# Kernel tuning notes

Measured on AMD Instinct MI355X. Metric: run time of the kernel, lower is better.

## Reference

```python
import jax, jax.numpy as jnp
import numpy as np

BETA = 0.25


def setup_inputs() -> dict:
    key = jax.random.key(0)
    k1, k2 = jax.random.split(key)
    z = jax.random.normal(k1, (16, 2048, 256), dtype=jnp.float32)
    # n_q=4 codebooks, each [n_e=2048, e_dim=256]; xavier-ish scale
    W = jax.random.normal(k2, (4, 2048, 256), dtype=jnp.float32) * 0.05
    return {"z": z, "W": W}


def reference(z, W):
    """Residual VQ forward (p=1.0, eval-mode math). Returns (z_q, loss, indices)."""
    n_q, n_e, e_dim = W.shape
    lead = z.shape[:-1]
    flat_shape = (-1, e_dim)

    residual = z
    cumulative_q = jnp.zeros_like(z)
    losses = []
    idx_list = []
    for k in range(n_q):
        Wk = W[k]  # [n_e, e_dim]
        flat = residual.reshape(flat_shape)  # [N, e_dim]
        dist = (
            jnp.sum(flat * flat, axis=1, keepdims=True)
            - 2.0 * (flat @ Wk.T)
            + jnp.sum(Wk * Wk, axis=1)[None, :]
        )
        idx = jnp.argmin(dist, axis=1)  # [N]
        # one_hot @ Wk is mathematically a gather of codebook rows
        q = Wk[idx].reshape(residual.shape)
        # commit + beta*codebook; both are (residual.detach() - q)^2.mean(-1)
        diff = jax.lax.stop_gradient(residual) - q
        losses.append((1.0 + BETA) * jnp.mean(diff * diff, axis=-1))
        cumulative_q = cumulative_q + q
        residual = residual - q
        idx_list.append(idx.reshape(*lead, 1))

    # straight-through: gradient of z_q flows only to z
    z_q = z + jax.lax.stop_gradient(cumulative_q - z)
    total_loss = jnp.mean(jnp.stack(losses, axis=0).mean(axis=0))
    indices = jnp.concatenate(idx_list, axis=-1)  # [..., n_q]
    return z_q, total_loss, indices
```

## Files before the change

kernel.cpp:

```cpp
#include <hip/hip_runtime.h>
#include <cstdint>
#include <math.h>
#include <float.h>

#define N_Q   4
#define NROWS 32768
#define EDIM  256
#define NE    2048
#define NCT   64
#define TM    64
#define NTHREADS 256

#define ZQ_SIZE  (NROWS * EDIM)
#define LOSS_OFF ZQ_SIZE
#define IDX_OFF  (ZQ_SIZE + 1)

#define TAU 0.012f

typedef __attribute__((ext_vector_type(8))) _Float16 f16x8;
typedef __attribute__((ext_vector_type(4))) float    f32x4;

union F8 { _Float16 h[8]; f16x8 v; };

__device__ __forceinline__ float np_block128_sq(const float* __restrict__ p) {
    #pragma clang fp contract(off)
    float r[8];
    #pragma unroll
    for (int j = 0; j < 8; ++j) { float v = p[j]; r[j] = v * v; }
    for (int i = 8; i < 128; i += 8) {
        #pragma unroll
        for (int j = 0; j < 8; ++j) { float v = p[i + j]; float sq = v * v; r[j] = r[j] + sq; }
    }
    return ((r[0] + r[1]) + (r[2] + r[3])) + ((r[4] + r[5]) + (r[6] + r[7]));
}

__global__ __launch_bounds__(256) void wsq_kernel(const float* __restrict__ W,
                                                  float* __restrict__ wsq32) {
    __shared__ float rowbuf[4][EDIM];
    int wv   = threadIdx.x >> 6;
    int row  = blockIdx.x * 4 + (threadIdx.x >> 6);
    int lane = threadIdx.x & 63;
    float4 v = ((const float4*)(W + (size_t)row * EDIM))[lane];
    *(float4*)&rowbuf[wv][lane * 4] = v;
    __syncthreads();
    if (lane == 0) {
        float a = np_block128_sq(rowbuf[wv]);
        float b = np_block128_sq(rowbuf[wv] + 128);
        wsq32[row] = a + b;
    }
}

__global__ __launch_bounds__(256) void wh_kernel(const float* __restrict__ W,
                                                 short* __restrict__ wh) {
    int gid  = blockIdx.x * 256 + threadIdx.x;
    int lane = gid & 63;
    int grp  = gid >> 6;
    int ctq  = grp >> 3;
    int ks   = grp & 7;
    int n = lane & 15, kq = lane >> 4;
    const float* src = W + (((size_t)(ctq * 16 + n)) << 8) + ks * 32 + kq * 8;
    float4 p0 = *(const float4*)src;
    float4 p1 = *(const float4*)(src + 4);
    float v[8] = {p0.x, p0.y, p0.z, p0.w, p1.x, p1.y, p1.z, p1.w};
    F8 h;
    #pragma unroll
    for (int j = 0; j < 8; ++j) h.h[j] = (_Float16)v[j];
    *(f16x8*)(wh + (((size_t)grp) << 9) + lane * 8) = h.v;
}

__device__ __forceinline__ void top3_merge(float& a1, int& ai1, float& a2, int& ai2, float& a3,
                                           float b1, int bi1, float b2, int bi2, float b3) {
    float c1, c2, c3; int k1, k2;
    if (b1 < a1 || (b1 == a1 && bi1 < ai1)) {
        c1 = b1; k1 = bi1;
        if (a1 < b2 || (a1 == b2 && ai1 < bi2)) { c2 = a1; k2 = ai1; c3 = fminf(b2, a2); }
        else                                    { c2 = b2; k2 = bi2; c3 = fminf(a1, b3); }
    } else {
        c1 = a1; k1 = ai1;
        if (b1 < a2 || (b1 == a2 && bi1 < ai2)) { c2 = b1; k2 = bi1; c3 = fminf(a2, b2); }
        else                                    { c2 = a2; k2 = ai2; c3 = fminf(b1, a3); }
    }
    a1 = c1; ai1 = k1; a2 = c2; ai2 = k2; a3 = c3;
}

__global__ __launch_bounds__(256, 2) void rvq_main(
    const float* __restrict__ z, const float* __restrict__ W,
    const float* __restrict__ wsq32, const short* __restrict__ wh,
    float* __restrict__ resd_g, float* __restrict__ out,
    float* __restrict__ loss_partial)
{
    __shared__ __align__(16) short lds_b[4][4][4][512];
    __shared__ float wsq_lds[2048];
    __shared__ float Srow[TM];
    __shared__ float rm1[2][TM], rm2[2][TM], rm3[2][TM];
    __shared__ int   ri1[2][TM], ri2[2][TM];
    __shared__ int   idx_s[TM], is2_s[TM];
    __shared__ int   rk_cnt, rk_list[TM];
    __shared__ int   pr_cnt, pr_list[TM];
    __shared__ float wavesum[4];

    float* rrow_s = (float*)&lds_b[0][0][0][0];
    float* red_f  = (float*)&lds_b[1][0][0][0];
    int*   red_i  = (int*)  &lds_b[1][1][0][0];

    const int tid  = threadIdx.x;
    const int wave = tid >> 6;
    const int lane = tid & 63;
    const int n    = lane & 15;
    const int kq   = lane >> 4;
    const int chalf = wave & 1;
    const int rsel  = wave >> 1;
    const int row0 = blockIdx.x * TM;
    const int rowg = row0 + rsel * 32;

    for (int i = tid; i < TM * 64; i += NTHREADS) {
        int r = i >> 6, c = i & 63;
        ((float4*)resd_g)[(((size_t)(row0 + r)) << 6) + c] =
            ((const float4*)z)[(((size_t)(row0 + r)) << 6) + c];
    }

    float lsum = 0.f;

    for (int q = 0; q < N_Q; ++q) {
        const float* Wk   = W + (size_t)q * NE * EDIM;
        const float* wsqk = wsq32 + q * NE;
        const short* whq  = wh + ((size_t)q << 19);

        __syncthreads();
        if (tid == 0) { rk_cnt = 0; pr_cnt = 0; }
        if (tid < 2 * TM) {
            int r = tid >> 1, hf = tid & 1;
            float s = np_block128_sq(resd_g + (((size_t)(row0 + r)) << 8) + hf * 128);
            float s2 = __shfl_xor(s, 1, 64);
            if (hf == 0) Srow[r] = s + s2;
        }
        for (int i = tid; i < 512; i += NTHREADS)
            ((float4*)wsq_lds)[i] = ((const float4*)wsqk)[i];

        f16x8 ah[2][8];
        #pragma unroll
        for (int t = 0; t < 2; ++t) {
            #pragma unroll
            for (int ks = 0; ks < 8; ++ks) {
                const float* rp = resd_g + (((size_t)(rowg + t * 16 + n)) << 8) + ks * 32 + kq * 8;
                float4 p0 = *(const float4*)rp;
                float4 p1 = *(const float4*)(rp + 4);
                float v[8] = {p0.x, p0.y, p0.z, p0.w, p1.x, p1.y, p1.z, p1.w};
                F8 h;
                #pragma unroll
                for (int j = 0; j < 8; ++j) h.h[j] = (_Float16)v[j];
                ah[t][ks] = h.v;
            }
        }
        __syncthreads();

        float M1[8], M2[8], M3[8]; int I1[8], I2[8];
        #pragma unroll
        for (int s = 0; s < 8; ++s) {
            M1[s] = INFINITY; M2[s] = INFINITY; M3[s] = INFINITY; I1[s] = 0; I2[s] = 0;
        }

        auto stage = [&](int p) {
            int ct = p >> 1, kp = p & 1;
            int b = p & 3;
            #pragma unroll
            for (int ksl = 0; ksl < 4; ++ksl) {
                size_t grp = ((size_t)(chalf * 64 + ct) << 3) + kp * 4 + ksl;
                const short* gp = whq + (grp << 9) + lane * 8;
                __builtin_amdgcn_global_load_lds(
                    (const __attribute__((address_space(1))) void*)gp,
                    (__attribute__((address_space(3))) void*)&lds_b[wave][b][ksl][0],
                    16, 0, 0);
            }
        };

        asm volatile("s_waitcnt vmcnt(0)" ::: "memory");
        stage(0);
        stage(1);

        f32x4 acc[2];
        for (int ct = 0; ct < NCT; ++ct) {
            float wq = wsq_lds[chalf * 1024 + ct * 16 + n];

            asm volatile("s_waitcnt vmcnt(4)" ::: "memory");
            __builtin_amdgcn_sched_barrier(0);
            {
                const int b = (2 * ct) & 3;
                acc[0] = (f32x4){0.f, 0.f, 0.f, 0.f};
                acc[1] = (f32x4){0.f, 0.f, 0.f, 0.f};
                #pragma unroll
                for (int ksl = 0; ksl < 4; ++ksl) {
                    f16x8 bh = *(const f16x8*)&lds_b[wave][b][ksl][lane * 8];
                    acc[0] = __builtin_amdgcn_mfma_f32_16x16x32_f16(ah[0][ksl], bh, acc[0], 0, 0, 0);
                    acc[1] = __builtin_amdgcn_mfma_f32_16x16x32_f16(ah[1][ksl], bh, acc[1], 0, 0, 0);
                }
            }
            if (ct < NCT - 1) stage(2 * ct + 2);

            if (ct < NCT - 1) {
                asm volatile("s_waitcnt vmcnt(4)" ::: "memory");
            } else {
                asm volatile("s_waitcnt vmcnt(0)" ::: "memory");
            }
            __builtin_amdgcn_sched_barrier(0);
            {
                const int b = (2 * ct + 1) & 3;
                #pragma unroll
                for (int ksl = 0; ksl < 4; ++ksl) {
                    f16x8 bh = *(const f16x8*)&lds_b[wave][b][ksl][lane * 8];
                    acc[0] = __builtin_amdgcn_mfma_f32_16x16x32_f16(ah[0][4 + ksl], bh, acc[0], 0, 0, 0);
                    acc[1] = __builtin_amdgcn_mfma_f32_16x16x32_f16(ah[1][4 + ksl], bh, acc[1], 0, 0, 0);
                }
            }
            if (ct < NCT - 1) stage(2 * ct + 3);

            int cg = chalf * 1024 + ct * 16 + n;
            #pragma unroll
            for (int t = 0; t < 2; ++t) {
                #pragma unroll
                for (int rg = 0; rg < 4; ++rg) {
                    float d = fmaf(-2.0f, acc[t][rg], wq);
                    int s = t * 4 + rg;
                    bool c1 = d < M1[s];
                    bool c2 = d < M2[s];
                    M3[s] = fminf(M3[s], fmaxf(M2[s], d));
                    M2[s] = fminf(M2[s], fmaxf(M1[s], d));
                    I2[s] = c1 ? I1[s] : (c2 ? cg : I2[s]);
                    M1[s] = fminf(M1[s], d);
                    I1[s] = c1 ? cg : I1[s];
                }
            }
        }

        #pragma unroll
        for (int s = 0; s < 8; ++s) {
            float a1 = M1[s], a2 = M2[s], a3 = M3[s]; int ai = I1[s], aj = I2[s];
            #pragma unroll
            for (int mask = 1; mask < 16; mask <<= 1) {
                float b1 = __shfl_xor(a1, mask, 64);
                float b2 = __shfl_xor(a2, mask, 64);
                float b3 = __shfl_xor(a3, mask, 64);
                int   bi = __shfl_xor(ai, mask, 64);
                int   bj = __shfl_xor(aj, mask, 64);
                top3_merge(a1, ai, a2, aj, a3, b1, bi, b2, bj, b3);
            }
            if (n == 0) {
                int rr = rsel * 32 + (s >> 2) * 16 + kq * 4 + (s & 3);
                rm1[chalf][rr] = a1; rm2[chalf][rr] = a2; rm3[chalf][rr] = a3;
                ri1[chalf][rr] = ai; ri2[chalf][rr] = aj;
            }
        }
        __syncthreads();

        if (tid < TM) {
            float a1 = rm1[0][tid], a2 = rm2[0][tid], a3 = rm3[0][tid];
            int ai = ri1[0][tid], aj = ri2[0][tid];
            top3_merge(a1, ai, a2, aj, a3,
                       rm1[1][tid], ri1[1][tid], rm2[1][tid], ri2[1][tid], rm3[1][tid]);
            idx_s[tid] = ai; is2_s[tid] = aj;
            if (a2 - a1 <= TAU) {
                if (a3 - a1 > TAU) { int p = atomicAdd(&pr_cnt, 1); pr_list[p] = tid; }
                else               { int p = atomicAdd(&rk_cnt, 1); rk_list[p] = tid; }
            }
        }
        __syncthreads();

        {
            int ncheck = rk_cnt;
            for (int f = 0; f < ncheck; ++f) {
                int r = rk_list[f];
                if (tid < 64)
                    ((float4*)rrow_s)[tid] =
                        ((const float4*)(resd_g + (((size_t)(row0 + r)) << 8)))[tid];
                __syncthreads();
                float Sr = Srow[r];
                float accv[8];
                #pragma unroll
                for (int j = 0; j < 8; ++j) accv[j] = 0.f;
                const float* wp = Wk + ((size_t)tid * 8) * EDIM;
                for (int kb = 0; kb < 64; ++kb) {
                    float4 rv = *(const float4*)&rrow_s[kb * 4];
                    #pragma unroll
                    for (int j = 0; j < 8; ++j) {
                        float4 wv = *(const float4*)(wp + j * EDIM + kb * 4);
                        accv[j] = fmaf(rv.x, wv.x, accv[j]);
                        accv[j] = fmaf(rv.y, wv.y, accv[j]);
                        accv[j] = fmaf(rv.z, wv.z, accv[j]);
                        accv[j] = fmaf(rv.w, wv.w, accv[j]);
                    }
                }
                float bm = FLT_MAX; int bi = 0;
                #pragma unroll
                for (int j = 0; j < 8; ++j) {
                    int c = tid * 8 + j;
                    float d = fmaf(-2.0f, accv[j], Sr) + wsqk[c];
                    if (d < bm) { bm = d; bi = c; }
                }
                red_f[tid] = bm; red_i[tid] = bi;
                __syncthreads();
                for (int off = 128; off > 0; off >>= 1) {
                    if (tid < off) {
                        float v = red_f[tid + off]; int ii = red_i[tid + off];
                        if (v < red_f[tid] || (v == red_f[tid] && ii < red_i[tid])) {
                            red_f[tid] = v; red_i[tid] = ii;
                        }
                    }
                    __syncthreads();
                }
                if (tid == 0) idx_s[r] = red_i[0];
                __syncthreads();
            }
        }

        {
            int cnt2 = pr_cnt * 2;
            for (int base = 0; base < cnt2; base += NTHREADS) {
                int slot = base + tid;
                float d = FLT_MAX; int code = 0; int r = -1;
                if (slot < cnt2) {
                    r = pr_list[slot >> 1];
                    code = (slot & 1) ? is2_s[r] : idx_s[r];
                    const float* rp = resd_g + (((size_t)(row0 + r)) << 8);
                    const float* wp = Wk + ((size_t)code << 8);
                    float acc1 = 0.f;
                    for (int kb = 0; kb < 64; ++kb) {
                        float4 rv = *(const float4*)(rp + kb * 4);
                        float4 wv = *(const float4*)(wp + kb * 4);
                        acc1 = fmaf(rv.x, wv.x, acc1);
                        acc1 = fmaf(rv.y, wv.y, acc1);
                        acc1 = fmaf(rv.z, wv.z, acc1);
                        acc1 = fmaf(rv.w, wv.w, acc1);
                    }
                    d = fmaf(-2.0f, acc1, Srow[r]) + wsqk[code];
                }
                float dp = __shfl_xor(d, 1, 64);
                int   cp = __shfl_xor(code, 1, 64);
                if (slot < cnt2 && (slot & 1) == 0) {
                    idx_s[r] = (dp < d || (dp == d && cp < code)) ? cp : code;
                }
            }
        }
        __syncthreads();

        if (tid < TM)
            out[IDX_OFF + (size_t)(row0 + tid) * N_Q + q] = (float)idx_s[tid];
        __syncthreads();

        {
            const int d = tid;
            for (int r = 0; r < TM; ++r) {
                float w = Wk[(((size_t)idx_s[r]) << 8) + d];
                float* rp = resd_g + (((size_t)(row0 + r)) << 8) + d;
                float nv = *rp - w;
                *rp = nv;
                lsum = fmaf(nv, nv, lsum);
            }
        }
    }

    __syncthreads();
    for (int i = tid; i < TM * 64; i += NTHREADS) {
        int r = i >> 6, c = i & 63;
        float4 zv = ((const float4*)z)[(((size_t)(row0 + r)) << 6) + c];
        float4 rv = ((const float4*)resd_g)[(((size_t)(row0 + r)) << 6) + c];
        float4 o = {zv.x - rv.x, zv.y - rv.y, zv.z - rv.z, zv.w - rv.w};
        ((float4*)out)[(((size_t)(row0 + r)) << 6) + c] = o;
    }
    #pragma unroll
    for (int off = 32; off > 0; off >>= 1) lsum += __shfl_down(lsum, off, 64);
    if (lane == 0) wavesum[wave] = lsum;
    __syncthreads();
    if (tid == 0)
        loss_partial[blockIdx.x] = wavesum[0] + wavesum[1] + wavesum[2] + wavesum[3];
}

__global__ __launch_bounds__(256) void loss_reduce(const float* __restrict__ partial,
                                                   float* __restrict__ out) {
    __shared__ float sh[256];
    int t = threadIdx.x;
    sh[t] = partial[t] + partial[t + 256];
    __syncthreads();
    for (int off = 128; off > 0; off >>= 1) {
        if (t < off) sh[t] += sh[t + off];
        __syncthreads();
    }
    if (t == 0)
        out[LOSS_OFF] = sh[0] * (1.25f / ((float)N_Q * (float)NROWS * (float)EDIM));
}

extern "C" void kernel_launch(void* const* d_in, const int* in_sizes, int n_in,
                              void* d_out, int out_size, void* d_ws, size_t ws_size,
                              hipStream_t stream) {
    const float* z = (const float*)d_in[0];
    const float* W = (const float*)d_in[1];
    float* out = (float*)d_out;

    float* wsq32   = (float*)d_ws;
    float* partial = (float*)((char*)d_ws + 32768);
    short* wh      = (short*)((char*)d_ws + 65536);
    float* resd    = (float*)((char*)d_ws + 65536 + 8388608);

    hipLaunchKernelGGL(wsq_kernel, dim3(NE * N_Q / 4), dim3(NTHREADS), 0, stream, W, wsq32);
    hipLaunchKernelGGL(wh_kernel, dim3(1024), dim3(NTHREADS), 0, stream, W, wh);
    hipLaunchKernelGGL(rvq_main, dim3(NROWS / TM), dim3(NTHREADS), 0, stream,
                       z, W, wsq32, wh, resd, out, partial);
    hipLaunchKernelGGL(loss_reduce, dim3(1), dim3(NTHREADS), 0, stream, partial, out);
}
```

Before: 592.0 us.

## Software-pipeline MFMA tiles with fold of previous tile and split accumulator chains

Restructures the codebook-tile loop so the MFMA compute for tile ct+1 is issued before the top-3 argmin fold of tile ct, using double-buffered accumulators. Each accumulator is also split into two independent chains (even/odd k-slices) that are summed before the distance compute, shortening MFMA dependency chains. This is meant to hide MFMA latency behind the VALU fold work. In exchange it doubles the accumulator registers, which may reduce occupancy or cause spills, and the split sum slightly changes fp32 rounding order.

New measurement: 752.2 us. 27.1% more time.

```diff
diff --git a/kernel.cpp b/kernel.cpp
--- a/kernel.cpp
+++ b/kernel.cpp
@@ -174,29 +174,25 @@
             }
         };
 
-        asm volatile("s_waitcnt vmcnt(0)" ::: "memory");
-        stage(0);
-        stage(1);
-
-        f32x4 acc[2];
-        for (int ct = 0; ct < NCT; ++ct) {
-            float wq = wsq_lds[chalf * 1024 + ct * 16 + n];
-
+        auto computeCT = [&](int ct, f32x4 (&acc)[2][2], float& wqv) {
+            wqv = wsq_lds[chalf * 1024 + ct * 16 + n];
             asm volatile("s_waitcnt vmcnt(4)" ::: "memory");
             __builtin_amdgcn_sched_barrier(0);
             {
                 const int b = (2 * ct) & 3;
-                acc[0] = (f32x4){0.f, 0.f, 0.f, 0.f};
-                acc[1] = (f32x4){0.f, 0.f, 0.f, 0.f};
+                acc[0][0] = (f32x4){0.f, 0.f, 0.f, 0.f};
+                acc[0][1] = (f32x4){0.f, 0.f, 0.f, 0.f};
+                acc[1][0] = (f32x4){0.f, 0.f, 0.f, 0.f};
+                acc[1][1] = (f32x4){0.f, 0.f, 0.f, 0.f};
                 #pragma unroll
                 for (int ksl = 0; ksl < 4; ++ksl) {
                     f16x8 bh = *(const f16x8*)&lds_b[wave][b][ksl][lane * 8];
-                    acc[0] = __builtin_amdgcn_mfma_f32_16x16x32_f16(ah[0][ksl], bh, acc[0], 0, 0, 0);
-                    acc[1] = __builtin_amdgcn_mfma_f32_16x16x32_f16(ah[1][ksl], bh, acc[1], 0, 0, 0);
-                }
-            }
-            if (ct < NCT - 1) stage(2 * ct + 2);
-
+                    const int c = ksl & 1;
+                    acc[0][c] = __builtin_amdgcn_mfma_f32_16x16x32_f16(ah[0][ksl], bh, acc[0][c], 0, 0, 0);
+                    acc[1][c] = __builtin_amdgcn_mfma_f32_16x16x32_f16(ah[1][ksl], bh, acc[1][c], 0, 0, 0);
+                }
+            }
+            if (2 * ct + 2 < 2 * NCT) stage(2 * ct + 2);
             if (ct < NCT - 1) {
                 asm volatile("s_waitcnt vmcnt(4)" ::: "memory");
             } else {
@@ -208,18 +204,22 @@
                 #pragma unroll
                 for (int ksl = 0; ksl < 4; ++ksl) {
                     f16x8 bh = *(const f16x8*)&lds_b[wave][b][ksl][lane * 8];
-                    acc[0] = __builtin_amdgcn_mfma_f32_16x16x32_f16(ah[0][4 + ksl], bh, acc[0], 0, 0, 0);
-                    acc[1] = __builtin_amdgcn_mfma_f32_16x16x32_f16(ah[1][4 + ksl], bh, acc[1], 0, 0, 0);
-                }
-            }
-            if (ct < NCT - 1) stage(2 * ct + 3);
-
+                    const int ks = 4 + ksl, c = ksl & 1;
+                    acc[0][c] = __builtin_amdgcn_mfma_f32_16x16x32_f16(ah[0][ks], bh, acc[0][c], 0, 0, 0);
+                    acc[1][c] = __builtin_amdgcn_mfma_f32_16x16x32_f16(ah[1][ks], bh, acc[1][c], 0, 0, 0);
+                }
+            }
+            if (2 * ct + 3 < 2 * NCT) stage(2 * ct + 3);
+        };
+
+        auto foldCT = [&](const f32x4 (&acc)[2][2], float wqv, int ct) {
             int cg = chalf * 1024 + ct * 16 + n;
             #pragma unroll
             for (int t = 0; t < 2; ++t) {
                 #pragma unroll
                 for (int rg = 0; rg < 4; ++rg) {
-                    float d = fmaf(-2.0f, acc[t][rg], wq);
+                    float g = acc[t][0][rg] + acc[t][1][rg];
+                    float d = fmaf(-2.0f, g, wqv);
                     int s = t * 4 + rg;
                     bool c1 = d < M1[s];
                     bool c2 = d < M2[s];
@@ -230,7 +230,24 @@
                     I1[s] = c1 ? cg : I1[s];
                 }
             }
-        }
+        };
+
+        asm volatile("s_waitcnt vmcnt(0)" ::: "memory");
+        stage(0);
+        stage(1);
+
+        f32x4 accE[2][2], accO[2][2];
+        float wqE, wqO;
+        computeCT(0, accE, wqE);
+        for (int ctp = 0; ctp < 31; ++ctp) {
+            computeCT(2 * ctp + 1, accO, wqO);
+            foldCT(accE, wqE, 2 * ctp);
+            computeCT(2 * ctp + 2, accE, wqE);
+            foldCT(accO, wqO, 2 * ctp + 1);
+        }
+        computeCT(63, accO, wqO);
+        foldCT(accE, wqE, 62);
+        foldCT(accO, wqO, 63);
 
         #pragma unroll
         for (int s = 0; s < 8; ++s) {
```
